# Performance work log

Measured on AMD Instinct MI355X. Metric: run time of the kernel, lower is better.

Reference implementation:

```python
import math
import jax, jax.numpy as jnp
import numpy as np

B, T, V, D, H = 4, 1024, 32000, 1024, 16
DK = D // H

def setup_inputs() -> dict:
    key = jax.random.key(0)
    ks = jax.random.split(key, 12)
    inputs = jax.random.randint(ks[0], (B, T), 0, V, dtype=jnp.int32)
    targets = jax.random.randint(ks[1], (B, T), 0, V, dtype=jnp.int32)
    tok_emb = jax.random.normal(ks[2], (V, D), dtype=jnp.float32) * 0.02
    pos_emb = jax.random.normal(ks[3], (T, D), dtype=jnp.float32) * 0.02
    s = 1.0 / math.sqrt(D)
    Wq = jax.random.normal(ks[4], (H, D, DK), dtype=jnp.float32) * s
    Wk = jax.random.normal(ks[5], (H, D, DK), dtype=jnp.float32) * s
    Wv = jax.random.normal(ks[6], (H, D, DK), dtype=jnp.float32) * s
    bq = jnp.zeros((H, DK), jnp.float32)
    bk = jnp.zeros((H, DK), jnp.float32)
    bv = jnp.zeros((H, DK), jnp.float32)
    Wo = jax.random.normal(ks[7], (D, V), dtype=jnp.float32) * s
    bo = jnp.zeros((V,), jnp.float32)
    return {"inputs": inputs, "targets": targets, "tok_emb": tok_emb, "pos_emb": pos_emb,
            "Wq": Wq, "bq": bq, "Wk": Wk, "bk": bk, "Wv": Wv, "bv": bv, "Wo": Wo, "bo": bo}

def reference(inputs, targets, tok_emb, pos_emb, Wq, bq, Wk, bk, Wv, bv, Wo, bo):
    Bc, Tc = inputs.shape
    d_model = tok_emb.shape[1]
    d_k = Wq.shape[-1]
    # embedding + positional encoding
    x = tok_emb[inputs] * math.sqrt(d_model) + pos_emb[:Tc][None]  # [B,T,D]
    # all heads' Q/K/V at once (original loops over heads)
    q = jnp.einsum('btd,hdk->bhtk', x, Wq) + bq[None, :, None, :]
    k = jnp.einsum('btd,hdk->bhtk', x, Wk) + bk[None, :, None, :]
    v = jnp.einsum('btd,hdk->bhtk', x, Wv) + bv[None, :, None, :]
    scores = jnp.einsum('bhtk,bhsk->bhts', q, k)
    causal = jnp.tril(jnp.ones((Tc, Tc), bool))
    # original masks with -1e9 BEFORE dividing by sqrt(d_k); replicate exactly
    scores = jnp.where(causal[None, None], scores, jnp.float32(-1e9))
    attn = jax.nn.softmax(scores / math.sqrt(d_k), axis=-1)
    out = jnp.einsum('bhts,bhsk->bhtk', attn, v)  # [B,H,T,dk]
    out = out.transpose(0, 2, 1, 3).reshape(Bc, Tc, d_model)  # concat heads
    logits = out @ Wo + bo  # [B,T,V]
    Vc = logits.shape[-1]
    logits = logits.reshape(Bc * Tc, Vc)
    tgt = targets.reshape(Bc * Tc)
    logp = jax.nn.log_softmax(logits, axis=-1)
    loss = -jnp.mean(jnp.take_along_axis(logp, tgt[:, None], axis=-1))
    return logits, loss
```

## Files before the change

### kernel.cpp

```cpp
#include <hip/hip_runtime.h>
#include <hip/hip_bf16.h>
#include <math.h>

#define B_  4
#define T_  1024
#define V_  32000
#define D_  1024
#define H_  16
#define DK_ 64
#define BT_ (B_*T_)

typedef unsigned short u16;
typedef short short8 __attribute__((ext_vector_type(8)));
typedef float f32x4 __attribute__((ext_vector_type(4)));

__device__ __forceinline__ float bf2f(u16 u) {
  union { unsigned int i; float f; } v; v.i = ((unsigned int)u) << 16; return v.f;
}
__device__ __forceinline__ u16 f2bf(float f) {
  union { float f; unsigned int i; } v; v.f = f;
  unsigned int x = v.i;
  return (u16)((x + 0x7fffu + ((x >> 16) & 1u)) >> 16);
}

__device__ __forceinline__ void gload16(const void* g, void* l) {
  __builtin_amdgcn_global_load_lds((const __attribute__((address_space(1))) void*)g,
                                   (__attribute__((address_space(3))) void*)l, 16, 0, 0);
}

__global__ void embed_kernel(const int* __restrict__ inputs, const float* __restrict__ tok_emb,
                             const float* __restrict__ pos_emb, u16* __restrict__ xb) {
  int row = blockIdx.x;
  int t = row & (T_ - 1);
  int tok = inputs[row];
  const float* te = tok_emb + (size_t)tok * D_;
  const float* pe = pos_emb + (size_t)t * D_;
  u16* out = xb + (size_t)row * D_;
  for (int d = threadIdx.x; d < D_; d += blockDim.x)
    out[d] = f2bf(te[d] * 32.0f + pe[d]);
}

__global__ void pack_w_kernel(const float* __restrict__ W, u16* __restrict__ Wt) {
  int n = blockIdx.x;
  int h = n >> 6, k = n & 63;
  const float* src = W + ((size_t)h * D_) * DK_ + k;
  u16* dst = Wt + (size_t)n * D_;
  for (int d = threadIdx.x; d < D_; d += blockDim.x)
    dst[d] = f2bf(src[(size_t)d * DK_]);
}

__global__ __launch_bounds__(256) void transpose_wo_kernel(const float* __restrict__ Wo,
                                                           u16* __restrict__ WoT) {
  __shared__ u16 tile[64][66];
  int n0 = blockIdx.x * 64;
  int d0 = blockIdx.y * 64;
  int tx = threadIdx.x & 63, ty = threadIdx.x >> 6;
  #pragma unroll
  for (int i = 0; i < 64; i += 4) {
    int d = d0 + ty + i;
    tile[ty + i][tx] = f2bf(Wo[(size_t)d * V_ + n0 + tx]);
  }
  __syncthreads();
  #pragma unroll
  for (int i = 0; i < 64; i += 4) {
    int n = n0 + ty + i;
    WoT[(size_t)n * D_ + d0 + tx] = tile[tx][ty + i];
  }
}

template<int MODE>
__global__ __launch_bounds__(256) void gemm_bt(const u16* __restrict__ A,
                                               const u16* __restrict__ Bt,
                                               const float* __restrict__ bias,
                                               void* __restrict__ Cout,
                                               int M, int N, int K) {
  __shared__ __align__(16) u16 As[128 * 32];
  __shared__ __align__(16) u16 Bs[128 * 32];
  int m0 = blockIdx.x * 128;
  int n0 = blockIdx.y * 128;
  int tid = threadIdx.x;
  int lane = tid & 63;
  int wave = tid >> 6;
  int wm = (wave >> 1) * 64, wn = (wave & 1) * 64;

  f32x4 acc[4][4] = {};

  int arow0 = tid >> 2;
  int acol  = (tid & 3) * 8;
  const u16* Ag = A  + (size_t)(m0 + arow0) * K + acol;
  const u16* Bg = Bt + (size_t)(n0 + arow0) * K + acol;
  u16* Asl = As + tid * 8;
  u16* Bsl = Bs + tid * 8;

  int fr = lane & 15;
  int fk = (lane >> 4) * 8;

  for (int k0 = 0; k0 < K; k0 += 32) {
    gload16(Ag + k0, Asl);
    gload16(Ag + (size_t)64 * K + k0, Asl + 2048);
    gload16(Bg + k0, Bsl);
    gload16(Bg + (size_t)64 * K + k0, Bsl + 2048);
    __syncthreads();
    short8 af[4], bfg[4];
    #pragma unroll
    for (int i = 0; i < 4; i++) {
      af[i]  = *(const short8*)(As + (wm + i * 16 + fr) * 32 + fk);
      bfg[i] = *(const short8*)(Bs + (wn + i * 16 + fr) * 32 + fk);
    }
    #pragma unroll
    for (int i = 0; i < 4; i++)
      #pragma unroll
      for (int j = 0; j < 4; j++)
        acc[i][j] = __builtin_amdgcn_mfma_f32_16x16x32_bf16(af[i], bfg[j], acc[i][j], 0, 0, 0);
    __syncthreads();
  }

  #pragma unroll
  for (int i = 0; i < 4; i++) {
    int rowb = m0 + wm + i * 16 + (lane >> 4) * 4;
    #pragma unroll
    for (int j = 0; j < 4; j++) {
      int n = n0 + wn + j * 16 + (lane & 15);
      float bv = bias[n];
      #pragma unroll
      for (int r = 0; r < 4; r++) {
        int m = rowb + r;
        float v = acc[i][j][r] + bv;
        if (MODE == 0) {
          ((float*)Cout)[(size_t)m * N + n] = v;
        } else {
          int b = m >> 10, t = m & 1023, h = n >> 6, k = n & 63;
          ((u16*)Cout)[((((size_t)b * H_ + h) * T_) + t) * DK_ + k] = f2bf(v);
        }
      }
    }
  }
}

__global__ __launch_bounds__(256) void flash_attn(const u16* __restrict__ Q,
                                                  const u16* __restrict__ Kw,
                                                  const u16* __restrict__ Vw,
                                                  u16* __restrict__ Oout) {
  int qt = blockIdx.x;
  int bh = blockIdx.y;
  int b = bh >> 4, h = bh & 15;
  const u16* Qb = Q  + (size_t)bh * T_ * DK_;
  const u16* Kb = Kw + (size_t)bh * T_ * DK_;
  const u16* Vb = Vw + (size_t)bh * T_ * DK_;
  int q0 = qt * 64;

  __shared__ __align__(16) u16 Qs[64 * 64];
  __shared__ __align__(16) u16 Ks[32 * 64];
  __shared__ __align__(16) u16 Vs[64 * 32];
  __shared__ __align__(16) u16 Ps[4][16 * 32];

  int tid = threadIdx.x, wave = tid >> 6, lane = tid & 63;
  int fr = lane & 15, fq = lane >> 4;

  {
    const u16* g = Qb + (size_t)(q0 + (tid >> 3)) * DK_ + (tid & 7) * 8;
    u16* l = Qs + tid * 8;
    gload16(g, l);
    gload16(g + 32 * DK_, l + 2048);
  }
  __syncthreads();
  short8 qf[2];
  #pragma unroll
  for (int c = 0; c < 2; c++)
    qf[c] = *(const short8*)(Qs + (wave * 16 + fr) * 64 + c * 32 + fq * 8);
  __syncthreads();

  float m_i[4], l_i[4];
  f32x4 o[4] = {};
  #pragma unroll
  for (int r = 0; r < 4; r++) { m_i[r] = -1e30f; l_i[r] = 0.f; }

  const float scale = 0.125f;
  int ntiles = (q0 + 63) / 32 + 1;

  for (int jt = 0; jt < ntiles; jt++) {
    int kb = jt * 32;
    gload16(Kb + (size_t)(kb + (tid >> 3)) * DK_ + (tid & 7) * 8, Ks + tid * 8);
    {
      int key = tid >> 3, d0v = (tid & 7) * 8;
      short8 vv = *(const short8*)(Vb + (size_t)(kb + key) * DK_ + d0v);
      #pragma unroll
      for (int j = 0; j < 8; j++)
        Vs[(d0v + j) * 32 + key] = ((const u16*)&vv)[j];
    }
    __syncthreads();

    short8 kf[2][2];
    #pragma unroll
    for (int t2 = 0; t2 < 2; t2++)
      #pragma unroll
      for (int c = 0; c < 2; c++)
        kf[t2][c] = *(const short8*)(Ks + (t2 * 16 + fr) * 64 + c * 32 + fq * 8);
    f32x4 zero = {0.f, 0.f, 0.f, 0.f};
    f32x4 s[2];
    #pragma unroll
    for (int t2 = 0; t2 < 2; t2++) {
      s[t2] = __builtin_amdgcn_mfma_f32_16x16x32_bf16(qf[0], kf[t2][0], zero, 0, 0, 0);
      s[t2] = __builtin_amdgcn_mfma_f32_16x16x32_bf16(qf[1], kf[t2][1], s[t2], 0, 0, 0);
    }

    float alpha_r[4], p0v[4], p1v[4];
    #pragma unroll
    for (int r = 0; r < 4; r++) {
      int qg = q0 + wave * 16 + fq * 4 + r;
      float s0 = s[0][r] * scale;
      float s1 = s[1][r] * scale;
      if (kb + fr > qg)      s0 = -1e30f;
      if (kb + 16 + fr > qg) s1 = -1e30f;
      float mx = fmaxf(s0, s1);
      mx = fmaxf(mx, __shfl_xor(mx, 1));
      mx = fmaxf(mx, __shfl_xor(mx, 2));
      mx = fmaxf(mx, __shfl_xor(mx, 4));
      mx = fmaxf(mx, __shfl_xor(mx, 8));
      float mn = fmaxf(m_i[r], mx);
      float p0 = __expf(s0 - mn), p1 = __expf(s1 - mn);
      float alpha = __expf(m_i[r] - mn);
      float psum = p0 + p1;
      psum += __shfl_xor(psum, 1);
      psum += __shfl_xor(psum, 2);
      psum += __shfl_xor(psum, 4);
      psum += __shfl_xor(psum, 8);
      l_i[r] = l_i[r] * alpha + psum;
      m_i[r] = mn;
      alpha_r[r] = alpha;
      p0v[r] = p0; p1v[r] = p1;
    }

    u16* Pw = Ps[wave];
    #pragma unroll
    for (int r = 0; r < 4; r++) {
      Pw[(fq * 4 + r) * 32 + fr]      = f2bf(p0v[r]);
      Pw[(fq * 4 + r) * 32 + 16 + fr] = f2bf(p1v[r]);
    }
    asm volatile("s_waitcnt lgkmcnt(0)" ::: "memory");
    short8 pf = *(const short8*)(Pw + fr * 32 + fq * 8);

    short8 vf[4];
    #pragma unroll
    for (int nt = 0; nt < 4; nt++)
      vf[nt] = *(const short8*)(Vs + (nt * 16 + fr) * 32 + fq * 8);

    #pragma unroll
    for (int nt = 0; nt < 4; nt++) {
      f32x4 c = o[nt];
      #pragma unroll
      for (int r = 0; r < 4; r++) c[r] *= alpha_r[r];
      o[nt] = __builtin_amdgcn_mfma_f32_16x16x32_bf16(pf, vf[nt], c, 0, 0, 0);
    }
    __syncthreads();
  }

  #pragma unroll
  for (int r = 0; r < 4; r++) l_i[r] = 1.0f / l_i[r];
  int trow = q0 + wave * 16 + fq * 4;
  #pragma unroll
  for (int nt = 0; nt < 4; nt++) {
    int d = h * 64 + nt * 16 + fr;
    #pragma unroll
    for (int r = 0; r < 4; r++) {
      int t = trow + r;
      Oout[((size_t)b * T_ + t) * D_ + d] = f2bf(o[nt][r] * l_i[r]);
    }
  }
}

__global__ __launch_bounds__(256) void row_loss_kernel(const float* __restrict__ logits,
                                                       const int* __restrict__ targets,
                                                       float* __restrict__ partial) {
  int row = blockIdx.x;
  const float* p = logits + (size_t)row * V_;
  __shared__ float red[256];
  float mx = -1e30f;
  for (int i = threadIdx.x; i < V_; i += 256) mx = fmaxf(mx, p[i]);
  red[threadIdx.x] = mx; __syncthreads();
  for (int s = 128; s > 0; s >>= 1) {
    if (threadIdx.x < s) red[threadIdx.x] = fmaxf(red[threadIdx.x], red[threadIdx.x + s]);
    __syncthreads();
  }
  mx = red[0]; __syncthreads();
  float sum = 0.f;
  for (int i = threadIdx.x; i < V_; i += 256) sum += __expf(p[i] - mx);
  red[threadIdx.x] = sum; __syncthreads();
  for (int s = 128; s > 0; s >>= 1) {
    if (threadIdx.x < s) red[threadIdx.x] += red[threadIdx.x + s];
    __syncthreads();
  }
  if (threadIdx.x == 0) {
    float lse = mx + __logf(red[0]);
    partial[row] = p[targets[row]] - lse;
  }
}

__global__ void final_loss_kernel(const float* __restrict__ partial, float* __restrict__ out_loss) {
  __shared__ float red[256];
  float s = 0.f;
  for (int i = threadIdx.x; i < BT_; i += 256) s += partial[i];
  red[threadIdx.x] = s; __syncthreads();
  for (int st = 128; st > 0; st >>= 1) {
    if (threadIdx.x < st) red[threadIdx.x] += red[threadIdx.x + st];
    __syncthreads();
  }
  if (threadIdx.x == 0) out_loss[0] = -red[0] / (float)BT_;
}

extern "C" void kernel_launch(void* const* d_in, const int* in_sizes, int n_in,
                              void* d_out, int out_size, void* d_ws, size_t ws_size,
                              hipStream_t stream) {
  const int*   inputs  = (const int*)d_in[0];
  const int*   targets = (const int*)d_in[1];
  const float* tok_emb = (const float*)d_in[2];
  const float* pos_emb = (const float*)d_in[3];
  const float* Wq = (const float*)d_in[4];
  const float* bq = (const float*)d_in[5];
  const float* Wk = (const float*)d_in[6];
  const float* bk = (const float*)d_in[7];
  const float* Wv = (const float*)d_in[8];
  const float* bv = (const float*)d_in[9];
  const float* Wo = (const float*)d_in[10];
  const float* bo = (const float*)d_in[11];

  char* w = (char*)d_ws;
  u16* xb   = (u16*)(w);
  u16* WqT  = (u16*)(w + 8388608);
  u16* WkT  = (u16*)(w + 10485760);
  u16* WvT  = (u16*)(w + 12582912);
  u16* WoT  = (u16*)(w + 14680064);
  u16* Qw   = (u16*)(w + 80216064);
  u16* Kw   = (u16*)(w + 88604672);
  u16* Vw   = (u16*)(w + 96993280);
  u16* AO   = (u16*)(w + 105381888);
  float* part = (float*)(w + 113770496);

  float* logits = (float*)d_out;
  float* loss   = logits + (size_t)BT_ * V_;

  embed_kernel<<<BT_, 256, 0, stream>>>(inputs, tok_emb, pos_emb, xb);
  pack_w_kernel<<<1024, 256, 0, stream>>>(Wq, WqT);
  pack_w_kernel<<<1024, 256, 0, stream>>>(Wk, WkT);
  pack_w_kernel<<<1024, 256, 0, stream>>>(Wv, WvT);
  transpose_wo_kernel<<<dim3(V_ / 64, D_ / 64), 256, 0, stream>>>(Wo, WoT);

  gemm_bt<1><<<dim3(BT_ / 128, D_ / 128), 256, 0, stream>>>(xb, WqT, bq, Qw, BT_, D_, D_);
  gemm_bt<1><<<dim3(BT_ / 128, D_ / 128), 256, 0, stream>>>(xb, WkT, bk, Kw, BT_, D_, D_);
  gemm_bt<1><<<dim3(BT_ / 128, D_ / 128), 256, 0, stream>>>(xb, WvT, bv, Vw, BT_, D_, D_);

  flash_attn<<<dim3(T_ / 64, B_ * H_), 256, 0, stream>>>(Qw, Kw, Vw, AO);

  gemm_bt<0><<<dim3(BT_ / 128, V_ / 128), 256, 0, stream>>>(AO, WoT, bo, (void*)logits, BT_, V_, D_);

  row_loss_kernel<<<BT_, 256, 0, stream>>>(logits, targets, part);
  final_loss_kernel<<<1, 256, 0, stream>>>(part, loss);
}
```

Measured before the change: 1.469 ms.

## Add 256x256-tile pipelined GEMM for output projection and single-pass online loss

Replaces the 128x128 output-projection GEMM with a dedicated 512-thread kernel that computes 256x256 tiles. It double-buffers LDS via direct global-to-LDS loads interleaved with MFMA quarters, uses s_setprio, and swizzles blocks for cache locality. The row-loss kernel becomes a single pass over float4-vectorized logits with an online max/sum-exp, so each row is read once instead of twice. The new GEMM hardcodes shapes and relies on a hand-tuned barrier/vmcnt schedule, which risks correctness or occupancy issues.

```diff
diff --git a/kernel.cpp b/kernel.cpp
--- a/kernel.cpp
+++ b/kernel.cpp
@@ -133,6 +133,125 @@
           ((u16*)Cout)[((((size_t)b * H_ + h) * T_) + t) * DK_ + k] = f2bf(v);
         }
       }
+    }
+  }
+}
+
+#define G256_NT 16
+#define G256_NB 125
+
+#define ISS(kt_, c_) do {                                                              \
+    const int kk_ = (((kt_) & (G256_NT - 1)) << 6);                                    \
+    const int pb_ = (kt_) & 1;                                                         \
+    const u16* s0_ = (((c_) < 2) ? Ab : Bb) + ((size_t)((((c_) & 1) << 7)) << 10) + kk_;\
+    u16* d0_ = &lds[pb_][((c_) < 2) ? 0 : 1][(((c_) & 1) ? 8192 : 0) + wl];            \
+    gload16(s0_, d0_);                                                                 \
+    gload16(s0_ + ((size_t)64 << 10), d0_ + 4096);                                     \
+  } while (0)
+
+#define MFMA_Q(MIOFF, NIOFF)                                                           \
+  __builtin_amdgcn_s_setprio(1);                                                       \
+  _Pragma("unroll")                                                                    \
+  for (int mi = 0; mi < 4; ++mi) {                                                     \
+    _Pragma("unroll")                                                                  \
+    for (int ni = 0; ni < 2; ++ni) {                                                   \
+      acc[(MIOFF)+mi][(NIOFF)+ni] = __builtin_amdgcn_mfma_f32_16x16x32_bf16(           \
+          Af[mi][0], Bf[(NIOFF)+ni][0], acc[(MIOFF)+mi][(NIOFF)+ni], 0, 0, 0);         \
+      acc[(MIOFF)+mi][(NIOFF)+ni] = __builtin_amdgcn_mfma_f32_16x16x32_bf16(           \
+          Af[mi][1], Bf[(NIOFF)+ni][1], acc[(MIOFF)+mi][(NIOFF)+ni], 0, 0, 0);         \
+    }                                                                                  \
+  }                                                                                    \
+  __builtin_amdgcn_s_setprio(0);
+
+__global__ __launch_bounds__(512, 2) void gemm256(const u16* __restrict__ A,
+                                                  const u16* __restrict__ Bt,
+                                                  const float* __restrict__ bias,
+                                                  float* __restrict__ C) {
+  __shared__ __align__(16) u16 lds[2][2][16384];
+
+  int bid = blockIdx.x;
+  int swz = (bid & 7) * (2000 / 8) + (bid >> 3);
+  int mb = swz / G256_NB, nb = swz % G256_NB;
+  int m0 = mb << 8, n0 = nb << 8;
+
+  const int tid = threadIdx.x;
+  const int w = tid >> 6, l = tid & 63;
+
+  const int rowS = ((w >> 1) << 4) + (l & 15);
+  const int kS   = ((w & 1) << 5) + ((l >> 4) << 3);
+  const int wl   = (w << 9) + (l << 3);
+
+  const u16* Ab = A  + ((size_t)(m0 + rowS) << 10) + kS;
+  const u16* Bb = Bt + ((size_t)(n0 + rowS) << 10) + kS;
+
+  f32x4 acc[8][4] = {};
+
+  ISS(0, 0); ISS(0, 1); ISS(0, 2); ISS(0, 3);
+  ISS(1, 0);
+  asm volatile("s_waitcnt vmcnt(2)" ::: "memory");
+  __builtin_amdgcn_s_barrier();
+
+  #pragma unroll 2
+  for (int kt = 0; kt < G256_NT; ++kt) {
+    const int p = kt & 1;
+    const u16* fA = &lds[p][0][((w >> 2) << 13) + (l << 3)];
+    const u16* fB = &lds[p][1][((w & 3) << 12) + (l << 3)];
+    short8 Af[4][2], Bf[4][2];
+
+    #pragma unroll
+    for (int mi = 0; mi < 4; ++mi)
+      #pragma unroll
+      for (int s = 0; s < 2; ++s)
+        Af[mi][s] = *(const short8*)(fA + ((mi * 2 + s) << 9));
+    #pragma unroll
+    for (int ni = 0; ni < 2; ++ni)
+      #pragma unroll
+      for (int s = 0; s < 2; ++s)
+        Bf[ni][s] = *(const short8*)(fB + ((ni * 2 + s) << 9));
+    ISS(kt + 1, 1);
+    __builtin_amdgcn_s_barrier();
+    MFMA_Q(0, 0)
+    __builtin_amdgcn_s_barrier();
+
+    #pragma unroll
+    for (int ni = 2; ni < 4; ++ni)
+      #pragma unroll
+      for (int s = 0; s < 2; ++s)
+        Bf[ni][s] = *(const short8*)(fB + ((ni * 2 + s) << 9));
+    ISS(kt + 1, 2);
+    __builtin_amdgcn_s_barrier();
+    MFMA_Q(0, 2)
+    __builtin_amdgcn_s_barrier();
+
+    #pragma unroll
+    for (int mi = 0; mi < 4; ++mi)
+      #pragma unroll
+      for (int s = 0; s < 2; ++s)
+        Af[mi][s] = *(const short8*)(fA + (((4 + mi) * 2 + s) << 9));
+    ISS(kt + 1, 3);
+    __builtin_amdgcn_s_barrier();
+    MFMA_Q(4, 0)
+    __builtin_amdgcn_s_barrier();
+
+    ISS(kt + 2, 0);
+    __builtin_amdgcn_s_barrier();
+    MFMA_Q(4, 2)
+    asm volatile("s_waitcnt vmcnt(2)" ::: "memory");
+    __builtin_amdgcn_s_barrier();
+  }
+
+  const int mrow = m0 + ((w >> 2) << 7) + ((l >> 4) << 2);
+  const int ncol = n0 + ((w & 3) << 6) + (l & 15);
+  #pragma unroll
+  for (int mi = 0; mi < 8; ++mi) {
+    #pragma unroll
+    for (int ni = 0; ni < 4; ++ni) {
+      const int n = ncol + ni * 16;
+      const float bv = bias[n];
+      float* Crow = C + (size_t)(mrow + mi * 16) * V_ + n;
+      #pragma unroll
+      for (int r = 0; r < 4; ++r)
+        Crow[(size_t)r * V_] = acc[mi][ni][r] + bv;
     }
   }
 }
@@ -273,26 +392,29 @@
                                                        const int* __restrict__ targets,
                                                        float* __restrict__ partial) {
   int row = blockIdx.x;
-  const float* p = logits + (size_t)row * V_;
-  __shared__ float red[256];
-  float mx = -1e30f;
-  for (int i = threadIdx.x; i < V_; i += 256) mx = fmaxf(mx, p[i]);
-  red[threadIdx.x] = mx; __syncthreads();
-  for (int s = 128; s > 0; s >>= 1) {
-    if (threadIdx.x < s) red[threadIdx.x] = fmaxf(red[threadIdx.x], red[threadIdx.x + s]);
-    __syncthreads();
-  }
-  mx = red[0]; __syncthreads();
-  float sum = 0.f;
-  for (int i = threadIdx.x; i < V_; i += 256) sum += __expf(p[i] - mx);
-  red[threadIdx.x] = sum; __syncthreads();
-  for (int s = 128; s > 0; s >>= 1) {
-    if (threadIdx.x < s) red[threadIdx.x] += red[threadIdx.x + s];
-    __syncthreads();
-  }
-  if (threadIdx.x == 0) {
-    float lse = mx + __logf(red[0]);
-    partial[row] = p[targets[row]] - lse;
+  int tid = threadIdx.x;
+  const float4* p4 = (const float4*)(logits + (size_t)row * V_);
+  float m = -1e30f, s = 0.f;
+  for (int i = tid; i < V_ / 4; i += 256) {
+    float4 v = p4[i];
+    float cm = fmaxf(fmaxf(v.x, v.y), fmaxf(v.z, v.w));
+    if (cm > m) { s *= __expf(m - cm); m = cm; }
+    s += __expf(v.x - m) + __expf(v.y - m) + __expf(v.z - m) + __expf(v.w - m);
+  }
+  __shared__ float rm[256], rs[256];
+  rm[tid] = m; rs[tid] = s; __syncthreads();
+  for (int st = 128; st > 0; st >>= 1) {
+    if (tid < st) {
+      float m2 = rm[tid + st], s2 = rs[tid + st];
+      float mn = fmaxf(rm[tid], m2);
+      rs[tid] = rs[tid] * __expf(rm[tid] - mn) + s2 * __expf(m2 - mn);
+      rm[tid] = mn;
+    }
+    __syncthreads();
+  }
+  if (tid == 0) {
+    float lse = rm[0] + __logf(rs[0]);
+    partial[row] = logits[(size_t)row * V_ + targets[row]] - lse;
   }
 }
 
@@ -351,7 +473,7 @@
 
   flash_attn<<<dim3(T_ / 64, B_ * H_), 256, 0, stream>>>(Qw, Kw, Vw, AO);
 
-  gemm_bt<0><<<dim3(BT_ / 128, V_ / 128), 256, 0, stream>>>(AO, WoT, bo, (void*)logits, BT_, V_, D_);
+  gemm256<<<(BT_ / 256) * (V_ / 256), 512, 0, stream>>>(AO, WoT, bo, logits);
 
   row_loss_kernel<<<BT_, 256, 0, stream>>>(logits, targets, part);
   final_loss_kernel<<<1, 256, 0, stream>>>(part, loss);
```

New measurement: 1.316 ms. 1.12x faster.
